# Performance work log

Hardware: AMD Instinct MI355X
Metric: run time of the kernel (lower is better)

## Reference

```python
import jax, jax.numpy as jnp
import numpy as np

N, IN_DIM, HIDDEN, L = 20000, 128, 256, 6
ALPHA = 0.1
EPS = 1e-5

def setup_inputs() -> dict:
    key = jax.random.key(0)
    ks = jax.random.split(key, 8)
    x = jax.random.normal(ks[0], (N, IN_DIM), dtype=jnp.float32)
    E = 320000
    src = jax.random.randint(ks[1], (E,), 0, N)
    dst = jax.random.randint(ks[2], (E,), 0, N)
    edge_index = jnp.stack([src, dst], axis=0)
    s = 1.0 / np.sqrt(IN_DIM)
    W_in = jax.random.normal(ks[3], (IN_DIM, HIDDEN), dtype=jnp.float32) * s
    b_in = jnp.zeros((HIDDEN,), dtype=jnp.float32)
    g_in = jnp.ones((HIDDEN,), dtype=jnp.float32)
    beta_in = jnp.zeros((HIDDEN,), dtype=jnp.float32)
    sc = 1.0 / np.sqrt(HIDDEN)
    Wc = jax.random.normal(ks[4], (L, HIDDEN, HIDDEN), dtype=jnp.float32) * sc
    bc = jnp.zeros((L, HIDDEN), dtype=jnp.float32)
    gc = jnp.ones((L, HIDDEN), dtype=jnp.float32)
    betac = jnp.zeros((L, HIDDEN), dtype=jnp.float32)
    return {"x": x, "edge_index": edge_index, "W_in": W_in, "b_in": b_in,
            "g_in": g_in, "beta_in": beta_in, "Wc": Wc, "bc": bc,
            "gc": gc, "betac": betac}

def _layer_norm(h, g, b):
    mu = jnp.mean(h, axis=-1, keepdims=True)
    var = jnp.mean((h - mu) ** 2, axis=-1, keepdims=True)
    return (h - mu) * jax.lax.rsqrt(var + EPS) * g + b

def _gcn_norm(edge_index, n):
    # add self loops (weight 1), symmetric normalization
    loop = jnp.arange(n, dtype=edge_index.dtype)
    row = jnp.concatenate([edge_index[0], loop])
    col = jnp.concatenate([edge_index[1], loop])
    w = jnp.ones((row.shape[0],), dtype=jnp.float32)
    deg = jax.ops.segment_sum(w, col, num_segments=n)
    dinv = jnp.where(deg > 0, jax.lax.rsqrt(deg), 0.0)
    norm = dinv[row] * w * dinv[col]
    return row, col, norm

def reference(x, edge_index, W_in, b_in, g_in, beta_in, Wc, bc, gc, betac):
    n = x.shape[0]
    row, col, norm = _gcn_norm(edge_index, n)
    # input block: Linear -> GELU -> LayerNorm (dropout = eval identity)
    h = _layer_norm(jax.nn.gelu(x @ W_in + b_in), g_in, beta_in)
    h0 = h
    xcur = h
    for l in range(L):
        z = xcur @ Wc[l]                              # [N, H]
        agg = jax.ops.segment_sum(z[row] * norm[:, None], col, num_segments=n)
        out = agg + bc[l]
        out = _layer_norm(jax.nn.gelu(out), gc[l], betac[l])
        hblend = (1.0 - ALPHA) * out + ALPHA * h0
        xcur = xcur + hblend
    return xcur
```

## Files before the change

kernel.cpp:

```cpp
#include <hip/hip_runtime.h>
#include <hip/hip_bf16.h>
#include <math.h>

#define HID 256
typedef __attribute__((ext_vector_type(8))) short s16x8;
typedef __attribute__((ext_vector_type(4))) float f32x4;

__device__ __forceinline__ ushort f2bf(float f){
    uint u = __float_as_uint(f);
    u += 0x7FFF + ((u>>16)&1);
    return (ushort)(u>>16);
}
__device__ __forceinline__ float bf2f(ushort b){
    return __uint_as_float(((uint)b)<<16);
}
__device__ __forceinline__ float4 bf4_to_f4(ushort4 u){
    return make_float4(bf2f(u.x), bf2f(u.y), bf2f(u.z), bf2f(u.w));
}

__device__ __forceinline__ float gelu_tanh(float x){
    float u = 0.7978845608028654f*(x + 0.044715f*x*x*x);
    float t = 1.0f - 2.0f/(1.0f + __expf(2.0f*u));
    return 0.5f*x*(1.0f+t);
}

__global__ void k_count(const int* __restrict__ dst, int* __restrict__ cnt, int E){
    int e = blockIdx.x*blockDim.x + threadIdx.x;
    if(e<E) atomicAdd(&cnt[dst[e]], 1);
}

__global__ __launch_bounds__(256) void k_scan1(const int* __restrict__ cnt,
    int* __restrict__ tsum, int* __restrict__ bsum, int N){
    __shared__ int sm[256];
    int t = threadIdx.x, b = blockIdx.x;
    int base = b*1024 + t*4;
    int c0=0,c1=0,c2=0,c3=0;
    if(base+3 < N){
        int4 c = *reinterpret_cast<const int4*>(&cnt[base]);
        c0=c.x; c1=c.y; c2=c.z; c3=c.w;
    }else{
        if(base  <N) c0=cnt[base];
        if(base+1<N) c1=cnt[base+1];
        if(base+2<N) c2=cnt[base+2];
        if(base+3<N) c3=cnt[base+3];
    }
    int s = c0+c1+c2+c3;
    sm[t]=s; __syncthreads();
    for(int off=1; off<256; off<<=1){
        int v = sm[t];
        int a = (t>=off)? sm[t-off] : 0;
        __syncthreads();
        sm[t] = v+a;
        __syncthreads();
    }
    tsum[b*256+t] = sm[t]-s;
    if(t==255) bsum[b] = sm[255];
}

__global__ void k_scan2(const int* __restrict__ bsum, int* __restrict__ boff,
    int* __restrict__ indptr, int B, int N){
    if(threadIdx.x==0 && blockIdx.x==0){
        int run=0;
        for(int i=0;i<B;i++){ boff[i]=run; run+=bsum[i]; }
        indptr[N]=run;
    }
}

__global__ __launch_bounds__(256) void k_scan3(const int* __restrict__ cnt,
    const int* __restrict__ tsum, const int* __restrict__ boff,
    int* __restrict__ indptr, int* __restrict__ cursor, float* __restrict__ dinv, int N){
    int t = threadIdx.x, b = blockIdx.x;
    int base = b*1024 + t*4;
    int run = boff[b] + tsum[b*256+t];
    #pragma unroll
    for(int i=0;i<4;i++){
        int idx = base+i;
        if(idx<N){
            int c = cnt[idx];
            indptr[idx]=run; cursor[idx]=run;
            dinv[idx] = rsqrtf((float)(c+1));
            run += c;
        }
    }
}

__global__ void k_fill(const int* __restrict__ src, const int* __restrict__ dst,
    int* __restrict__ cursor, int* __restrict__ csr, int E){
    int e = blockIdx.x*blockDim.x + threadIdx.x;
    if(e<E){
        int pos = atomicAdd(&cursor[dst[e]], 1);
        csr[pos] = src[e];
    }
}

__global__ void k_cvt_win(const float* __restrict__ W, ushort* __restrict__ Wb){
    int i = blockIdx.x*blockDim.x + threadIdx.x;
    if(i >= 128*256) return;
    int k = i >> 8, n = i & 255;
    int kb = k>>5, hi=(k>>3)&3, ii=k&7;
    Wb[((kb*256+n)*4+hi)*8 + ii] = f2bf(W[i]);
}
__global__ void k_cvt_wc(const float* __restrict__ W, ushort* __restrict__ Wb){
    int i = blockIdx.x*blockDim.x + threadIdx.x;
    if(i >= 6*65536) return;
    int l = i >> 16;
    int k = (i>>8)&255, n = i&255;
    int kb = k>>5, hi=(k>>3)&3, ii=k&7;
    Wb[l*65536 + ((kb*256+n)*4+hi)*8 + ii] = f2bf(W[i]);
}

__global__ __launch_bounds__(256) void k_agg(const ushort* __restrict__ xsc,
    const int* __restrict__ indptr, const int* __restrict__ csr,
    const float* __restrict__ dinv, ushort* __restrict__ yb, int N)
{
    int wave = threadIdx.x>>6, lane = threadIdx.x&63;
    int n = blockIdx.x*4 + wave;
    if(n>=N) return;
    const ushort4* X4 = reinterpret_cast<const ushort4*>(xsc);
    float4 acc = bf4_to_f4(X4[(size_t)n*64+lane]);
    int e0 = indptr[n], e1 = indptr[n+1];
    int e = e0;
    for(; e+8<=e1; e+=8){
        int idx[8];
        #pragma unroll
        for(int q=0;q<8;q++) idx[q]=csr[e+q];
        float4 v[8];
        #pragma unroll
        for(int q=0;q<8;q++) v[q]=bf4_to_f4(X4[(size_t)idx[q]*64+lane]);
        #pragma unroll
        for(int q=0;q<8;q++){
            acc.x+=v[q].x; acc.y+=v[q].y; acc.z+=v[q].z; acc.w+=v[q].w;
        }
    }
    if(e+4<=e1){
        int i0=csr[e], i1=csr[e+1], i2=csr[e+2], i3=csr[e+3];
        float4 v0 = bf4_to_f4(X4[(size_t)i0*64+lane]);
        float4 v1 = bf4_to_f4(X4[(size_t)i1*64+lane]);
        float4 v2 = bf4_to_f4(X4[(size_t)i2*64+lane]);
        float4 v3 = bf4_to_f4(X4[(size_t)i3*64+lane]);
        acc.x += (v0.x+v1.x)+(v2.x+v3.x);
        acc.y += (v0.y+v1.y)+(v2.y+v3.y);
        acc.z += (v0.z+v1.z)+(v2.z+v3.z);
        acc.w += (v0.w+v1.w)+(v2.w+v3.w);
        e += 4;
    }
    for(; e<e1; e++){
        float4 v = bf4_to_f4(X4[(size_t)csr[e]*64+lane]);
        acc.x+=v.x; acc.y+=v.y; acc.z+=v.z; acc.w+=v.w;
    }
    float dn = dinv[n];
    ushort4 o; o.x=f2bf(dn*acc.x); o.y=f2bf(dn*acc.y); o.z=f2bf(dn*acc.z); o.w=f2bf(dn*acc.w);
    reinterpret_cast<ushort4*>(yb)[(size_t)n*64+lane] = o;
}

template<bool INPUT>
__device__ __forceinline__ void epilogue16(f32x4 (&acc)[4],
    const float* __restrict__ bp, const float* __restrict__ gp, const float* __restrict__ bep,
    const float* __restrict__ dinv, ushort* __restrict__ h0b,
    float* __restrict__ xcur, ushort* __restrict__ xs_out,
    int row0, int wc, int lr, int hi, int N,
    float (*sm1)[4], float (*sm2)[4])
{
    float bcv[4], gcv[4], bev[4];
    #pragma unroll
    for(int nf=0;nf<4;nf++){
        int col = wc*64 + nf*16 + lr;
        bcv[nf]=bp[col]; gcv[nf]=gp[col]; bev[nf]=bep[col];
    }
    #pragma unroll
    for(int r=0;r<4;r++){
        float ls1=0.f, ls2=0.f;
        #pragma unroll
        for(int nf=0;nf<4;nf++){
            float t = gelu_tanh(acc[nf][r] + bcv[nf]);
            acc[nf][r] = t;
            ls1 += t; ls2 += t*t;
        }
        #pragma unroll
        for(int off=1; off<16; off<<=1){
            ls1 += __shfl_xor(ls1, off, 64);
            ls2 += __shfl_xor(ls2, off, 64);
        }
        if(lr==0){
            int row = hi*4 + r;
            sm1[row][wc]=ls1; sm2[row][wc]=ls2;
        }
    }
    __syncthreads();
    #pragma unroll
    for(int r=0;r<4;r++){
        int row = hi*4 + r;
        int grow = row0 + row;
        if(grow >= N) continue;
        float S1 = sm1[row][0]+sm1[row][1]+sm1[row][2]+sm1[row][3];
        float S2 = sm2[row][0]+sm2[row][1]+sm2[row][2]+sm2[row][3];
        float mu = S1*(1.0f/256.0f);
        float var = fmaxf(S2*(1.0f/256.0f) - mu*mu, 0.0f);
        float rs = rsqrtf(var + 1e-5f);
        float dv = dinv[grow];
        #pragma unroll
        for(int nf=0;nf<4;nf++){
            int col = wc*64 + nf*16 + lr;
            size_t idx = (size_t)grow*HID + col;
            float o = (acc[nf][r]-mu)*rs*gcv[nf] + bev[nf];
            if(INPUT){
                h0b[idx] = f2bf(o);
                xcur[idx] = o;
                xs_out[idx] = f2bf(dv*o);
            }else{
                float h = bf2f(h0b[idx]);
                float xc = xcur[idx] + 0.9f*o + 0.1f*h;
                xcur[idx] = xc;
                xs_out[idx] = f2bf(dv*xc);
            }
        }
    }
}

__global__ __launch_bounds__(256) void k_gemm_in(const float* __restrict__ X,
    const ushort* __restrict__ Wb,
    const float* __restrict__ bp, const float* __restrict__ gp, const float* __restrict__ bep,
    const float* __restrict__ dinv, ushort* __restrict__ h0b,
    float* __restrict__ xcur, ushort* __restrict__ xs_out, int N)
{
    const int lane = threadIdx.x & 63;
    const int wc = threadIdx.x >> 6;
    const int lr = lane & 15;
    const int hi = lane >> 4;
    const int row0 = blockIdx.x*16;
    __shared__ float sm1[16][4];
    __shared__ float sm2[16][4];

    f32x4 acc[4];
    #pragma unroll
    for(int n=0;n<4;n++){ acc[n].x=0.f; acc[n].y=0.f; acc[n].z=0.f; acc[n].w=0.f; }

    int r0 = row0 + lr; if(r0 >= N) r0 = N-1;
    const float* xp0 = X + (size_t)r0*128 + hi*8;
    const ushort* bpp = Wb + (wc*64 + lr)*32 + hi*8;

    #pragma unroll
    for(int kb=0; kb<4; kb++){
        float4 p0a = *reinterpret_cast<const float4*>(xp0 + kb*32);
        float4 p0b = *reinterpret_cast<const float4*>(xp0 + kb*32 + 4);
        s16x8 a0;
        a0[0]=(short)f2bf(p0a.x); a0[1]=(short)f2bf(p0a.y); a0[2]=(short)f2bf(p0a.z); a0[3]=(short)f2bf(p0a.w);
        a0[4]=(short)f2bf(p0b.x); a0[5]=(short)f2bf(p0b.y); a0[6]=(short)f2bf(p0b.z); a0[7]=(short)f2bf(p0b.w);
        #pragma unroll
        for(int nf=0;nf<4;nf++){
            s16x8 b = *reinterpret_cast<const s16x8*>(bpp + kb*8192 + nf*512);
            acc[nf] = __builtin_amdgcn_mfma_f32_16x16x32_bf16(a0, b, acc[nf], 0,0,0);
        }
    }
    epilogue16<true>(acc, bp, gp, bep, dinv, h0b, xcur, xs_out, row0, wc, lr, hi, N, sm1, sm2);
}

__global__ __launch_bounds__(256) void k_gemm_fused(const ushort* __restrict__ A,
    const ushort* __restrict__ Wb,
    const float* __restrict__ bp, const float* __restrict__ gp, const float* __restrict__ bep,
    const float* __restrict__ dinv, ushort* __restrict__ h0b,
    float* __restrict__ xcur, ushort* __restrict__ xs_out, int N)
{
    const int lane = threadIdx.x & 63;
    const int wc = threadIdx.x >> 6;
    const int lr = lane & 15;
    const int hi = lane >> 4;
    const int row0 = blockIdx.x*16;
    __shared__ float sm1[16][4];
    __shared__ float sm2[16][4];

    f32x4 acc[4];
    #pragma unroll
    for(int n=0;n<4;n++){ acc[n].x=0.f; acc[n].y=0.f; acc[n].z=0.f; acc[n].w=0.f; }

    int r0 = row0 + lr; if(r0 >= N) r0 = N-1;
    const ushort* ap0 = A + (size_t)r0*256 + hi*8;
    const ushort* bpp = Wb + (wc*64 + lr)*32 + hi*8;

    s16x8 a0[2], bb[2][4];
    a0[0] = *reinterpret_cast<const s16x8*>(ap0);
    #pragma unroll
    for(int nf=0;nf<4;nf++) bb[0][nf] = *reinterpret_cast<const s16x8*>(bpp + nf*512);

    #pragma unroll
    for(int kb=0; kb<8; kb++){
        const int cur = kb&1, nxt = cur^1;
        if(kb < 7){
            a0[nxt] = *reinterpret_cast<const s16x8*>(ap0 + (kb+1)*32);
            #pragma unroll
            for(int nf=0;nf<4;nf++)
                bb[nxt][nf] = *reinterpret_cast<const s16x8*>(bpp + (kb+1)*8192 + nf*512);
        }
        #pragma unroll
        for(int nf=0;nf<4;nf++)
            acc[nf] = __builtin_amdgcn_mfma_f32_16x16x32_bf16(a0[cur], bb[cur][nf], acc[nf], 0,0,0);
    }
    epilogue16<false>(acc, bp, gp, bep, dinv, h0b, xcur, xs_out, row0, wc, lr, hi, N, sm1, sm2);
}

extern "C" void kernel_launch(void* const* d_in, const int* in_sizes, int n_in,
                              void* d_out, int out_size, void* d_ws, size_t ws_size,
                              hipStream_t stream){
    const float* x     = (const float*)d_in[0];
    const int*   ei    = (const int*)d_in[1];
    const float* W_in  = (const float*)d_in[2];
    const float* b_in  = (const float*)d_in[3];
    const float* g_in  = (const float*)d_in[4];
    const float* be_in = (const float*)d_in[5];
    const float* Wc    = (const float*)d_in[6];
    const float* bc    = (const float*)d_in[7];
    const float* gc    = (const float*)d_in[8];
    const float* bec   = (const float*)d_in[9];
    const int N = in_sizes[0]/128;
    const int E = in_sizes[1]/2;
    const int* src = ei;
    const int* dst = ei + E;
    float* xcur = (float*)d_out;
    const int B = (N+1023)/1024;

    char* w = (char*)d_ws;
    ushort* xsc  = (ushort*)w; w += (size_t)N*HID*2;
    ushort* yb   = (ushort*)w; w += (size_t)N*HID*2;
    ushort* h0b  = (ushort*)w; w += (size_t)N*HID*2;
    ushort* wbin = (ushort*)w; w += (size_t)128*256*2;
    ushort* wbc  = (ushort*)w; w += (size_t)6*65536*2;
    float* dinv  = (float*)w;  w += (size_t)N*4;
    int* cnt     = (int*)w;    w += (size_t)N*4;
    int* cursor  = (int*)w;    w += (size_t)N*4;
    int* csr     = (int*)w;    w += (size_t)E*4;
    int* indptr  = (int*)w;    w += (size_t)(N+1)*4;
    int* tsum    = (int*)w;    w += (size_t)B*256*4;
    int* bsum    = (int*)w;    w += (size_t)B*4;
    int* boff    = (int*)w;    w += (size_t)B*4;

    (void)hipMemsetAsync(cnt, 0, (size_t)N*4, stream);
    k_count<<<(E+255)/256,256,0,stream>>>(dst,cnt,E);
    k_scan1<<<B,256,0,stream>>>(cnt, tsum, bsum, N);
    k_scan2<<<1,64,0,stream>>>(bsum, boff, indptr, B, N);
    k_scan3<<<B,256,0,stream>>>(cnt, tsum, boff, indptr, cursor, dinv, N);
    k_fill<<<(E+255)/256,256,0,stream>>>(src,dst,cursor,csr,E);

    k_cvt_win<<<(128*256+255)/256,256,0,stream>>>(W_in, wbin);
    k_cvt_wc<<<(6*65536+255)/256,256,0,stream>>>(Wc, wbc);

    const int GB = (N+15)/16;
    k_gemm_in<<<GB,256,0,stream>>>(x, wbin, b_in, g_in, be_in, dinv, h0b, xcur, xsc, N);
    for(int l=0;l<6;l++){
        k_agg<<<(N+3)/4,256,0,stream>>>(xsc, indptr, csr, dinv, yb, N);
        k_gemm_fused<<<GB,256,0,stream>>>(yb, wbc+(size_t)l*65536,
            bc+(size_t)l*HID, gc+(size_t)l*HID, bec+(size_t)l*HID,
            dinv, h0b, xcur, xsc, N);
    }
}
```

Measured before the change: 351.7 us.

## Keep running state in bf16, apply source dinv in aggregation, merge setup kernels

The running residual xcur is now stored only as bf16 in the workspace instead of an fp32 copy plus a dinv-prescaled bf16 copy. The fp32 output is written only in the last layer. The per-source dinv scaling moves from the GEMM epilogue into the aggregation gather, which adds a dinv load per edge. The scan2 kernel is folded into scan3 and the two weight-conversion kernels are merged, cutting launches. The intent is to reduce epilogue memory traffic per layer, at the cost of bf16 rounding accumulating in the residual across layers and extra scattered dinv reads.

```diff
diff --git a/kernel.cpp b/kernel.cpp
--- a/kernel.cpp
+++ b/kernel.cpp
@@ -57,21 +57,21 @@
     if(t==255) bsum[b] = sm[255];
 }
 
-__global__ void k_scan2(const int* __restrict__ bsum, int* __restrict__ boff,
-    int* __restrict__ indptr, int B, int N){
-    if(threadIdx.x==0 && blockIdx.x==0){
-        int run=0;
-        for(int i=0;i<B;i++){ boff[i]=run; run+=bsum[i]; }
-        indptr[N]=run;
-    }
-}
-
 __global__ __launch_bounds__(256) void k_scan3(const int* __restrict__ cnt,
-    const int* __restrict__ tsum, const int* __restrict__ boff,
-    int* __restrict__ indptr, int* __restrict__ cursor, float* __restrict__ dinv, int N){
+    const int* __restrict__ tsum, const int* __restrict__ bsum,
+    int* __restrict__ indptr, int* __restrict__ cursor, float* __restrict__ dinv,
+    int N, int B){
+    __shared__ int sboff, stot;
     int t = threadIdx.x, b = blockIdx.x;
+    if(t==0){
+        int run=0, tot=0;
+        for(int i=0;i<B;i++){ int v=bsum[i]; if(i<b) run+=v; tot+=v; }
+        sboff=run; stot=tot;
+        if(b==0) indptr[N]=tot;
+    }
+    __syncthreads();
     int base = b*1024 + t*4;
-    int run = boff[b] + tsum[b*256+t];
+    int run = sboff + tsum[b*256+t];
     #pragma unroll
     for(int i=0;i<4;i++){
         int idx = base+i;
@@ -93,71 +93,76 @@
     }
 }
 
-__global__ void k_cvt_win(const float* __restrict__ W, ushort* __restrict__ Wb){
+__global__ void k_cvt_w(const float* __restrict__ Win, const float* __restrict__ Wc,
+    ushort* __restrict__ wbin, ushort* __restrict__ wbc){
     int i = blockIdx.x*blockDim.x + threadIdx.x;
-    if(i >= 128*256) return;
-    int k = i >> 8, n = i & 255;
-    int kb = k>>5, hi=(k>>3)&3, ii=k&7;
-    Wb[((kb*256+n)*4+hi)*8 + ii] = f2bf(W[i]);
-}
-__global__ void k_cvt_wc(const float* __restrict__ W, ushort* __restrict__ Wb){
-    int i = blockIdx.x*blockDim.x + threadIdx.x;
-    if(i >= 6*65536) return;
-    int l = i >> 16;
-    int k = (i>>8)&255, n = i&255;
-    int kb = k>>5, hi=(k>>3)&3, ii=k&7;
-    Wb[l*65536 + ((kb*256+n)*4+hi)*8 + ii] = f2bf(W[i]);
-}
-
-__global__ __launch_bounds__(256) void k_agg(const ushort* __restrict__ xsc,
+    if(i < 32768){
+        int k = i >> 8, n = i & 255;
+        int kb = k>>5, hi=(k>>3)&3, ii=k&7;
+        wbin[((kb*256+n)*4+hi)*8 + ii] = f2bf(Win[i]);
+    }else if(i < 32768 + 6*65536){
+        int j = i - 32768;
+        int l = j >> 16;
+        int k = (j>>8)&255, n = j&255;
+        int kb = k>>5, hi=(k>>3)&3, ii=k&7;
+        wbc[l*65536 + ((kb*256+n)*4+hi)*8 + ii] = f2bf(Wc[j]);
+    }
+}
+
+__global__ __launch_bounds__(256) void k_agg(const ushort* __restrict__ xb,
     const int* __restrict__ indptr, const int* __restrict__ csr,
     const float* __restrict__ dinv, ushort* __restrict__ yb, int N)
 {
     int wave = threadIdx.x>>6, lane = threadIdx.x&63;
     int n = blockIdx.x*4 + wave;
     if(n>=N) return;
-    const ushort4* X4 = reinterpret_cast<const ushort4*>(xsc);
-    float4 acc = bf4_to_f4(X4[(size_t)n*64+lane]);
+    const ushort4* X4 = reinterpret_cast<const ushort4*>(xb);
+    float dn = dinv[n];
+    float4 sv = bf4_to_f4(X4[(size_t)n*64+lane]);
+    float4 acc = make_float4(dn*sv.x, dn*sv.y, dn*sv.z, dn*sv.w);
     int e0 = indptr[n], e1 = indptr[n+1];
     int e = e0;
     for(; e+8<=e1; e+=8){
         int idx[8];
         #pragma unroll
         for(int q=0;q<8;q++) idx[q]=csr[e+q];
-        float4 v[8];
-        #pragma unroll
-        for(int q=0;q<8;q++) v[q]=bf4_to_f4(X4[(size_t)idx[q]*64+lane]);
+        float4 v[8]; float dv[8];
+        #pragma unroll
+        for(int q=0;q<8;q++){ v[q]=bf4_to_f4(X4[(size_t)idx[q]*64+lane]); dv[q]=dinv[idx[q]]; }
         #pragma unroll
         for(int q=0;q<8;q++){
-            acc.x+=v[q].x; acc.y+=v[q].y; acc.z+=v[q].z; acc.w+=v[q].w;
+            acc.x = fmaf(dv[q],v[q].x,acc.x);
+            acc.y = fmaf(dv[q],v[q].y,acc.y);
+            acc.z = fmaf(dv[q],v[q].z,acc.z);
+            acc.w = fmaf(dv[q],v[q].w,acc.w);
         }
     }
     if(e+4<=e1){
         int i0=csr[e], i1=csr[e+1], i2=csr[e+2], i3=csr[e+3];
-        float4 v0 = bf4_to_f4(X4[(size_t)i0*64+lane]);
-        float4 v1 = bf4_to_f4(X4[(size_t)i1*64+lane]);
-        float4 v2 = bf4_to_f4(X4[(size_t)i2*64+lane]);
-        float4 v3 = bf4_to_f4(X4[(size_t)i3*64+lane]);
-        acc.x += (v0.x+v1.x)+(v2.x+v3.x);
-        acc.y += (v0.y+v1.y)+(v2.y+v3.y);
-        acc.z += (v0.z+v1.z)+(v2.z+v3.z);
-        acc.w += (v0.w+v1.w)+(v2.w+v3.w);
+        float4 v0 = bf4_to_f4(X4[(size_t)i0*64+lane]); float d0=dinv[i0];
+        float4 v1 = bf4_to_f4(X4[(size_t)i1*64+lane]); float d1=dinv[i1];
+        float4 v2 = bf4_to_f4(X4[(size_t)i2*64+lane]); float d2=dinv[i2];
+        float4 v3 = bf4_to_f4(X4[(size_t)i3*64+lane]); float d3=dinv[i3];
+        acc.x += d0*v0.x + d1*v1.x + d2*v2.x + d3*v3.x;
+        acc.y += d0*v0.y + d1*v1.y + d2*v2.y + d3*v3.y;
+        acc.z += d0*v0.z + d1*v1.z + d2*v2.z + d3*v3.z;
+        acc.w += d0*v0.w + d1*v1.w + d2*v2.w + d3*v3.w;
         e += 4;
     }
     for(; e<e1; e++){
-        float4 v = bf4_to_f4(X4[(size_t)csr[e]*64+lane]);
-        acc.x+=v.x; acc.y+=v.y; acc.z+=v.z; acc.w+=v.w;
-    }
-    float dn = dinv[n];
+        int s = csr[e];
+        float4 v = bf4_to_f4(X4[(size_t)s*64+lane]); float d=dinv[s];
+        acc.x = fmaf(d,v.x,acc.x); acc.y = fmaf(d,v.y,acc.y);
+        acc.z = fmaf(d,v.z,acc.z); acc.w = fmaf(d,v.w,acc.w);
+    }
     ushort4 o; o.x=f2bf(dn*acc.x); o.y=f2bf(dn*acc.y); o.z=f2bf(dn*acc.z); o.w=f2bf(dn*acc.w);
     reinterpret_cast<ushort4*>(yb)[(size_t)n*64+lane] = o;
 }
 
-template<bool INPUT>
+template<int MODE>
 __device__ __forceinline__ void epilogue16(f32x4 (&acc)[4],
     const float* __restrict__ bp, const float* __restrict__ gp, const float* __restrict__ bep,
-    const float* __restrict__ dinv, ushort* __restrict__ h0b,
-    float* __restrict__ xcur, ushort* __restrict__ xs_out,
+    ushort* __restrict__ h0b, ushort* __restrict__ xb, float* __restrict__ fout,
     int row0, int wc, int lr, int hi, int N,
     float (*sm1)[4], float (*sm2)[4])
 {
@@ -197,21 +202,19 @@
         float mu = S1*(1.0f/256.0f);
         float var = fmaxf(S2*(1.0f/256.0f) - mu*mu, 0.0f);
         float rs = rsqrtf(var + 1e-5f);
-        float dv = dinv[grow];
         #pragma unroll
         for(int nf=0;nf<4;nf++){
             int col = wc*64 + nf*16 + lr;
             size_t idx = (size_t)grow*HID + col;
             float o = (acc[nf][r]-mu)*rs*gcv[nf] + bev[nf];
-            if(INPUT){
-                h0b[idx] = f2bf(o);
-                xcur[idx] = o;
-                xs_out[idx] = f2bf(dv*o);
+            if(MODE==0){
+                ushort ob = f2bf(o);
+                h0b[idx] = ob;
+                xb[idx] = ob;
             }else{
-                float h = bf2f(h0b[idx]);
-                float xc = xcur[idx] + 0.9f*o + 0.1f*h;
-                xcur[idx] = xc;
-                xs_out[idx] = f2bf(dv*xc);
+                float xc = bf2f(xb[idx]) + 0.9f*o + 0.1f*bf2f(h0b[idx]);
+                if(MODE==1) xb[idx] = f2bf(xc);
+                else        fout[idx] = xc;
             }
         }
     }
@@ -220,8 +223,7 @@
 __global__ __launch_bounds__(256) void k_gemm_in(const float* __restrict__ X,
     const ushort* __restrict__ Wb,
     const float* __restrict__ bp, const float* __restrict__ gp, const float* __restrict__ bep,
-    const float* __restrict__ dinv, ushort* __restrict__ h0b,
-    float* __restrict__ xcur, ushort* __restrict__ xs_out, int N)
+    ushort* __restrict__ h0b, ushort* __restrict__ xb, int N)
 {
     const int lane = threadIdx.x & 63;
     const int wc = threadIdx.x >> 6;
@@ -252,14 +254,14 @@
             acc[nf] = __builtin_amdgcn_mfma_f32_16x16x32_bf16(a0, b, acc[nf], 0,0,0);
         }
     }
-    epilogue16<true>(acc, bp, gp, bep, dinv, h0b, xcur, xs_out, row0, wc, lr, hi, N, sm1, sm2);
-}
-
+    epilogue16<0>(acc, bp, gp, bep, h0b, xb, nullptr, row0, wc, lr, hi, N, sm1, sm2);
+}
+
+template<int MODE>
 __global__ __launch_bounds__(256) void k_gemm_fused(const ushort* __restrict__ A,
     const ushort* __restrict__ Wb,
     const float* __restrict__ bp, const float* __restrict__ gp, const float* __restrict__ bep,
-    const float* __restrict__ dinv, ushort* __restrict__ h0b,
-    float* __restrict__ xcur, ushort* __restrict__ xs_out, int N)
+    ushort* __restrict__ h0b, ushort* __restrict__ xb, float* __restrict__ fout, int N)
 {
     const int lane = threadIdx.x & 63;
     const int wc = threadIdx.x >> 6;
@@ -295,7 +297,7 @@
         for(int nf=0;nf<4;nf++)
             acc[nf] = __builtin_amdgcn_mfma_f32_16x16x32_bf16(a0[cur], bb[cur][nf], acc[nf], 0,0,0);
     }
-    epilogue16<false>(acc, bp, gp, bep, dinv, h0b, xcur, xs_out, row0, wc, lr, hi, N, sm1, sm2);
+    epilogue16<MODE>(acc, bp, gp, bep, h0b, xb, fout, row0, wc, lr, hi, N, sm1, sm2);
 }
 
 extern "C" void kernel_launch(void* const* d_in, const int* in_sizes, int n_in,
@@ -315,11 +317,11 @@
     const int E = in_sizes[1]/2;
     const int* src = ei;
     const int* dst = ei + E;
-    float* xcur = (float*)d_out;
+    float* fout = (float*)d_out;
     const int B = (N+1023)/1024;
 
     char* w = (char*)d_ws;
-    ushort* xsc  = (ushort*)w; w += (size_t)N*HID*2;
+    ushort* xb   = (ushort*)w; w += (size_t)N*HID*2;
     ushort* yb   = (ushort*)w; w += (size_t)N*HID*2;
     ushort* h0b  = (ushort*)w; w += (size_t)N*HID*2;
     ushort* wbin = (ushort*)w; w += (size_t)128*256*2;
@@ -331,24 +333,25 @@
     int* indptr  = (int*)w;    w += (size_t)(N+1)*4;
     int* tsum    = (int*)w;    w += (size_t)B*256*4;
     int* bsum    = (int*)w;    w += (size_t)B*4;
-    int* boff    = (int*)w;    w += (size_t)B*4;
 
     (void)hipMemsetAsync(cnt, 0, (size_t)N*4, stream);
     k_count<<<(E+255)/256,256,0,stream>>>(dst,cnt,E);
     k_scan1<<<B,256,0,stream>>>(cnt, tsum, bsum, N);
-    k_scan2<<<1,64,0,stream>>>(bsum, boff, indptr, B, N);
-    k_scan3<<<B,256,0,stream>>>(cnt, tsum, boff, indptr, cursor, dinv, N);
+    k_scan3<<<B,256,0,stream>>>(cnt, tsum, bsum, indptr, cursor, dinv, N, B);
     k_fill<<<(E+255)/256,256,0,stream>>>(src,dst,cursor,csr,E);
-
-    k_cvt_win<<<(128*256+255)/256,256,0,stream>>>(W_in, wbin);
-    k_cvt_wc<<<(6*65536+255)/256,256,0,stream>>>(Wc, wbc);
+    k_cvt_w<<<(32768+6*65536+255)/256,256,0,stream>>>(W_in, Wc, wbin, wbc);
 
     const int GB = (N+15)/16;
-    k_gemm_in<<<GB,256,0,stream>>>(x, wbin, b_in, g_in, be_in, dinv, h0b, xcur, xsc, N);
+    k_gemm_in<<<GB,256,0,stream>>>(x, wbin, b_in, g_in, be_in, h0b, xb, N);
     for(int l=0;l<6;l++){
-        k_agg<<<(N+3)/4,256,0,stream>>>(xsc, indptr, csr, dinv, yb, N);
-        k_gemm_fused<<<GB,256,0,stream>>>(yb, wbc+(size_t)l*65536,
-            bc+(size_t)l*HID, gc+(size_t)l*HID, bec+(size_t)l*HID,
-            dinv, h0b, xcur, xsc, N);
-    }
-}
+        k_agg<<<(N+3)/4,256,0,stream>>>(xb, indptr, csr, dinv, yb, N);
+        if(l<5)
+            k_gemm_fused<1><<<GB,256,0,stream>>>(yb, wbc+(size_t)l*65536,
+                bc+(size_t)l*HID, gc+(size_t)l*HID, bec+(size_t)l*HID,
+                h0b, xb, nullptr, N);
+        else
+            k_gemm_fused<2><<<GB,256,0,stream>>>(yb, wbc+(size_t)l*65536,
+                bc+(size_t)l*HID, gc+(size_t)l*HID, bec+(size_t)l*HID,
+                h0b, xb, fout, N);
+    }
+}
```

New measurement: 336.1 us. 1.05x faster.
